# Performance work log

Hardware: AMD Instinct MI355X
Metric: run time of the kernel (lower is better)

Reference implementation:

```python
import jax, jax.numpy as jnp
import numpy as np

B, C, H, W = 512, 128, 7, 7
P = 21            # patch_size
DIL = 2           # dilation_patch
PAD = DIL * (P // 2)  # 20: max displacement in pixels


def setup_inputs() -> dict:
    key = jax.random.key(0)
    k1, k2, k3, k4 = jax.random.split(key, 4)
    patch1 = jax.random.normal(k1, (B, C, H, W), jnp.float32)
    patch2 = jax.random.normal(k2, (B, C, H, W), jnp.float32)
    feat = P * P * H * W  # 21609
    w_bbox = jax.random.normal(k3, (4, feat), jnp.float32) * (1.0 / np.sqrt(feat))
    b_bbox = jax.random.normal(k4, (4,), jnp.float32) * 0.01
    return {"patch1": patch1, "patch2": patch2, "w_bbox": w_bbox, "b_bbox": b_bbox}


def _correlation(patch1, patch2):
    """SpatialCorrelationSampler(patch_size=21, dilation_patch=2, kernel_size=1).

    out[b,p,q,i,j] = sum_c patch1[b,c,i,j] * patch2[b,c, i + 2*(p-10), j + 2*(q-10)]
    with zero padding for out-of-bounds displacements. Output: [B, 21, 21, 7, 7].
    """
    padded = jnp.pad(patch2, ((0, 0), (0, 0), (PAD, PAD), (PAD, PAD)))  # [B,C,47,47]
    # Outer product over spatial positions, contracted over channels:
    # T[b,i,j,u,v] = sum_c patch1[b,c,i,j] * padded[b,c,u,v]
    T = jnp.einsum('bcij,bcuv->bijuv', patch1, padded)  # [B,7,7,47,47]
    # Gather the displaced entries: u = 2p + i, v = 2q + j
    Pp, Qq, Ii, Jj = jnp.meshgrid(jnp.arange(P), jnp.arange(P),
                                  jnp.arange(H), jnp.arange(W), indexing='ij')
    corr = T[:, Ii, Jj, DIL * Pp + Ii, DIL * Qq + Jj]  # [B,21,21,7,7]
    return corr


def reference(patch1, patch2, w_bbox, b_bbox):
    corr = _correlation(patch1, patch2)           # [B,21,21,7,7]
    x = corr.reshape(corr.shape[0], -1)           # flatten(start_dim=1)
    return x @ w_bbox.T + b_bbox                  # [B,4]
```

## Files before the change

kernel.cpp:

```cpp
#include <hip/hip_runtime.h>

#define NB    512
#define NC    128
#define HW    49
#define FEAT  21609
#define CHW   6272
#define NV4   1568
#define TSTR  132

__constant__ int c_S[7] = {0, 4, 7, 11, 14, 18, 21};

__global__ __launch_bounds__(256) void corr_head_kernel(
    const float* __restrict__ patch1,
    const float* __restrict__ patch2,
    const float* __restrict__ w_bbox,
    const float* __restrict__ b_bbox,
    float* __restrict__ out)
{
    __shared__ float  s1t[HW * TSTR];
    __shared__ float  s2t[HW * TSTR];
    __shared__ float4 s_w[625];
    __shared__ float  s_red[16];

    const int tid = threadIdx.x;
    const int b   = blockIdx.x;

    if (tid < 49) {
        int i  = tid / 7, j = tid - 7 * i;
        int ci = 4 - (i & 1);
        int n  = c_S[i] * 25 + ci * c_S[j];
        for (int i2 = (i & 1); i2 < 7; i2 += 2) {
            for (int j2 = (j & 1); j2 < 7; j2 += 2) {
                int p = 10 + ((i2 - i) >> 1);
                int q = 10 + ((j2 - j) >> 1);
                int f = ((p * 21 + q) * 7 + i) * 7 + j;
                s_w[n] = make_float4(w_bbox[f], w_bbox[FEAT + f],
                                     w_bbox[2 * FEAT + f], w_bbox[3 * FEAT + f]);
                ++n;
            }
        }
    }

    const float4* g1 = (const float4*)(patch1 + (size_t)b * CHW);
    const float4* g2 = (const float4*)(patch2 + (size_t)b * CHW);
    for (int t = tid; t < NV4; t += 256) {
        float4 v = g1[t];
        int e = t * 4;
        #pragma unroll
        for (int k = 0; k < 4; ++k) {
            int ee = e + k;
            int c  = ee / 49;
            int ij = ee - 49 * c;
            s1t[ij * TSTR + c] = (&v.x)[k];
        }
    }
    for (int t = tid; t < NV4; t += 256) {
        float4 v = g2[t];
        int e = t * 4;
        #pragma unroll
        for (int k = 0; k < 4; ++k) {
            int ee = e + k;
            int c  = ee / 49;
            int ij = ee - 49 * c;
            s2t[ij * TSTR + c] = (&v.x)[k];
        }
    }
    __syncthreads();

    const int p  = tid >> 5;
    const int co = (tid & 31) * 4;
    float a0 = 0.f, a1 = 0.f, a2 = 0.f, a3 = 0.f;

    for (int ij = p; ij < 49; ij += 8) {
        int i = ij / 7, j = ij - 7 * i;
        const float4 f1 = *(const float4*)(s1t + ij * TSTR + co);
        int ci = 4 - (i & 1);
        int n  = c_S[i] * 25 + ci * c_S[j];
        for (int i2 = (i & 1); i2 < 7; i2 += 2) {
            const float* rowb = s2t + (i2 * 7) * TSTR + co;
            for (int j2 = (j & 1); j2 < 7; j2 += 2) {
                const float4 f2 = *(const float4*)(rowb + j2 * TSTR);
                float4 w4 = s_w[n];
                ++n;
                float s = f1.x * f2.x + f1.y * f2.y + f1.z * f2.z + f1.w * f2.w;
                a0 = fmaf(s, w4.x, a0);
                a1 = fmaf(s, w4.y, a1);
                a2 = fmaf(s, w4.z, a2);
                a3 = fmaf(s, w4.w, a3);
            }
        }
    }

    for (int off = 32; off > 0; off >>= 1) {
        a0 += __shfl_down(a0, off, 64);
        a1 += __shfl_down(a1, off, 64);
        a2 += __shfl_down(a2, off, 64);
        a3 += __shfl_down(a3, off, 64);
    }
    if ((tid & 63) == 0) {
        int w = tid >> 6;
        s_red[w * 4 + 0] = a0;
        s_red[w * 4 + 1] = a1;
        s_red[w * 4 + 2] = a2;
        s_red[w * 4 + 3] = a3;
    }
    __syncthreads();
    if (tid < 4) {
        float r = s_red[tid] + s_red[4 + tid] + s_red[8 + tid] + s_red[12 + tid];
        out[b * 4 + tid] = r + b_bbox[tid];
    }
}

extern "C" void kernel_launch(void* const* d_in, const int* in_sizes, int n_in,
                              void* d_out, int out_size, void* d_ws, size_t ws_size,
                              hipStream_t stream) {
    const float* patch1 = (const float*)d_in[0];
    const float* patch2 = (const float*)d_in[1];
    const float* w_bbox = (const float*)d_in[2];
    const float* b_bbox = (const float*)d_in[3];
    float* out = (float*)d_out;
    corr_head_kernel<<<dim3(NB), dim3(256), 0, stream>>>(patch1, patch2, w_bbox, b_bbox, out);
}
```

Baseline: 88.60 us.

## Restructure correlation into parity-split planes with bf16 patch1 and weights

Changes how patch2 is laid out in shared memory: it is split into even/odd column planes padded to a 4x4 grid per channel, so each thread handles one output position and a quarter of the channels and computes 16 displacement dot products with vector loads. patch1 and the bbox weights are rounded to bf16 in shared memory, cutting LDS footprint, and the weight table is padded to 16 entries per position so the inner loop has no branches. The change trades exact fp32 accuracy for lower shared-memory traffic and better occupancy, and only 196 of the 256 threads do the main compute.

```diff
diff --git a/kernel.cpp b/kernel.cpp
--- a/kernel.cpp
+++ b/kernel.cpp
@@ -1,14 +1,19 @@
 #include <hip/hip_runtime.h>
 
 #define NB    512
-#define NC    128
-#define HW    49
 #define FEAT  21609
 #define CHW   6272
 #define NV4   1568
-#define TSTR  132
+#define PLANE 5120
 
-__constant__ int c_S[7] = {0, 4, 7, 11, 14, 18, 21};
+__device__ __forceinline__ unsigned short f2bf(float x) {
+    unsigned u = __float_as_uint(x);
+    u += 0x7fffu + ((u >> 16) & 1u);
+    return (unsigned short)(u >> 16);
+}
+__device__ __forceinline__ float bf2f(unsigned short h) {
+    return __uint_as_float((unsigned)h << 16);
+}
 
 __global__ __launch_bounds__(256) void corr_head_kernel(
     const float* __restrict__ patch1,
@@ -17,78 +22,99 @@
     const float* __restrict__ b_bbox,
     float* __restrict__ out)
 {
-    __shared__ float  s1t[HW * TSTR];
-    __shared__ float  s2t[HW * TSTR];
-    __shared__ float4 s_w[625];
-    __shared__ float  s_red[16];
+    __shared__ __align__(16) unsigned short s1b[CHW];
+    __shared__ __align__(16) float          s2p[2 * PLANE];
+    __shared__ __align__(16) ushort4        s_wq[784];
+    __shared__ float s_red[16];
 
     const int tid = threadIdx.x;
     const int b   = blockIdx.x;
 
-    if (tid < 49) {
-        int i  = tid / 7, j = tid - 7 * i;
-        int ci = 4 - (i & 1);
-        int n  = c_S[i] * 25 + ci * c_S[j];
-        for (int i2 = (i & 1); i2 < 7; i2 += 2) {
-            for (int j2 = (j & 1); j2 < 7; j2 += 2) {
-                int p = 10 + ((i2 - i) >> 1);
-                int q = 10 + ((j2 - j) >> 1);
-                int f = ((p * 21 + q) * 7 + i) * 7 + j;
-                s_w[n] = make_float4(w_bbox[f], w_bbox[FEAT + f],
-                                     w_bbox[2 * FEAT + f], w_bbox[3 * FEAT + f]);
-                ++n;
-            }
+    for (int n = tid; n < 1024; n += 256) {
+        int jp = n >> 9, c = (n >> 2) & 127, u = n & 3;
+        s2p[jp * PLANE + c * 40 + 28 + u] = 0.f;
+    }
+    for (int n = tid; n < 896; n += 256) {
+        int c = n / 7, i2 = n - 7 * c;
+        s2p[PLANE + c * 40 + i2 * 4 + 3] = 0.f;
+    }
+
+    const float4* g1 = (const float4*)(patch1 + (size_t)b * CHW);
+    for (int t = tid; t < NV4; t += 256) {
+        float4 v = g1[t];
+        ((ushort4*)s1b)[t] = make_ushort4(f2bf(v.x), f2bf(v.y), f2bf(v.z), f2bf(v.w));
+    }
+
+    const float4* g2 = (const float4*)(patch2 + (size_t)b * CHW);
+    for (int t = tid; t < NV4; t += 256) {
+        float4 v = g2[t];
+        int e = t * 4;
+        int c = e / 49;
+        int r = e - 49 * c;
+        #pragma unroll
+        for (int k = 0; k < 4; ++k) {
+            int i2 = (r * 37) >> 8;
+            int j2 = r - 7 * i2;
+            s2p[(j2 & 1) * PLANE + c * 40 + i2 * 4 + (j2 >> 1)] = (&v.x)[k];
+            if (++r == 49) { r = 0; ++c; }
         }
     }
 
-    const float4* g1 = (const float4*)(patch1 + (size_t)b * CHW);
-    const float4* g2 = (const float4*)(patch2 + (size_t)b * CHW);
-    for (int t = tid; t < NV4; t += 256) {
-        float4 v = g1[t];
-        int e = t * 4;
-        #pragma unroll
-        for (int k = 0; k < 4; ++k) {
-            int ee = e + k;
-            int c  = ee / 49;
-            int ij = ee - 49 * c;
-            s1t[ij * TSTR + c] = (&v.x)[k];
+    for (int n = tid; n < 784; n += 256) {
+        int ij = n % 49, tu = n / 49;
+        int t = tu >> 2, u = tu & 3;
+        int i = ij / 7, j = ij - 7 * i;
+        int i2 = (i & 1) + 2 * t, j2 = (j & 1) + 2 * u;
+        ushort4 wq = make_ushort4(0, 0, 0, 0);
+        if (i2 < 7 && j2 < 7) {
+            int p = 10 + ((i2 - i) >> 1);
+            int q = 10 + ((j2 - j) >> 1);
+            int f = ((p * 21 + q) * 7 + i) * 7 + j;
+            wq = make_ushort4(f2bf(w_bbox[f]), f2bf(w_bbox[FEAT + f]),
+                              f2bf(w_bbox[2 * FEAT + f]), f2bf(w_bbox[3 * FEAT + f]));
         }
-    }
-    for (int t = tid; t < NV4; t += 256) {
-        float4 v = g2[t];
-        int e = t * 4;
-        #pragma unroll
-        for (int k = 0; k < 4; ++k) {
-            int ee = e + k;
-            int c  = ee / 49;
-            int ij = ee - 49 * c;
-            s2t[ij * TSTR + c] = (&v.x)[k];
-        }
+        s_wq[n] = wq;
     }
     __syncthreads();
 
-    const int p  = tid >> 5;
-    const int co = (tid & 31) * 4;
     float a0 = 0.f, a1 = 0.f, a2 = 0.f, a3 = 0.f;
+    if (tid < 196) {
+        const int ij = tid >> 2, cs = tid & 3;
+        const int i = ij / 7, j = ij - 7 * i;
+        const float* base2 = s2p + (j & 1) * PLANE + (i & 1) * 4;
 
-    for (int ij = p; ij < 49; ij += 8) {
-        int i = ij / 7, j = ij - 7 * i;
-        const float4 f1 = *(const float4*)(s1t + ij * TSTR + co);
-        int ci = 4 - (i & 1);
-        int n  = c_S[i] * 25 + ci * c_S[j];
-        for (int i2 = (i & 1); i2 < 7; i2 += 2) {
-            const float* rowb = s2t + (i2 * 7) * TSTR + co;
-            for (int j2 = (j & 1); j2 < 7; j2 += 2) {
-                const float4 f2 = *(const float4*)(rowb + j2 * TSTR);
-                float4 w4 = s_w[n];
-                ++n;
-                float s = f1.x * f2.x + f1.y * f2.y + f1.z * f2.z + f1.w * f2.w;
-                a0 = fmaf(s, w4.x, a0);
-                a1 = fmaf(s, w4.y, a1);
-                a2 = fmaf(s, w4.z, a2);
-                a3 = fmaf(s, w4.w, a3);
+        float dot[4][4];
+        #pragma unroll
+        for (int t = 0; t < 4; ++t)
+            #pragma unroll
+            for (int u = 0; u < 4; ++u) dot[t][u] = 0.f;
+
+        #pragma unroll 2
+        for (int cc = 0; cc < 32; ++cc) {
+            int c = cs + 4 * cc;
+            float f1 = bf2f(s1b[c * 49 + ij]);
+            const float* bc = base2 + c * 40;
+            #pragma unroll
+            for (int t = 0; t < 4; ++t) {
+                float4 f2 = *(const float4*)(bc + 8 * t);
+                dot[t][0] = fmaf(f1, f2.x, dot[t][0]);
+                dot[t][1] = fmaf(f1, f2.y, dot[t][1]);
+                dot[t][2] = fmaf(f1, f2.z, dot[t][2]);
+                dot[t][3] = fmaf(f1, f2.w, dot[t][3]);
             }
         }
+
+        #pragma unroll
+        for (int t = 0; t < 4; ++t)
+            #pragma unroll
+            for (int u = 0; u < 4; ++u) {
+                ushort4 wq = s_wq[(4 * t + u) * 49 + ij];
+                float d = dot[t][u];
+                a0 = fmaf(d, bf2f(wq.x), a0);
+                a1 = fmaf(d, bf2f(wq.y), a1);
+                a2 = fmaf(d, bf2f(wq.z), a2);
+                a3 = fmaf(d, bf2f(wq.w), a3);
+            }
     }
 
     for (int off = 32; off > 0; off >>= 1) {
```

After: 80.65 us. -9.0%, faster.
